# Kernel tuning notes

Hardware: AMD Instinct MI355X
Metric: run time of the kernel (lower is better)

The kernel has to match this reference:

```python
import jax, jax.numpy as jnp
import numpy as np


def setup_inputs() -> dict:
    key = jax.random.key(0)
    k1, k2 = jax.random.split(key)
    label = jax.random.normal(k1, (8, 19, 320, 2048), dtype=jnp.float32)
    energy = jax.random.normal(k2, (8, 1280, 1280), dtype=jnp.float32)
    return {"label": label, "energy": energy}


def reference(label, energy):
    b, c, h, w = label.shape
    # log_softmax over channel dim (as in original)
    ls = jax.nn.log_softmax(label, axis=1)
    hh, ww = h // 16, w // 16
    # AdaptiveAvgPool2d((h/16, w/16)) with divisible dims == exact 16x16 block mean
    pooled = ls.reshape(b, c, hh, 16, ww, 16).mean(axis=(3, 5))  # [b,c,hh,ww]
    lab = jnp.argmax(pooled, axis=1)            # [b,hh,ww]
    lab = lab[:, 10:20, :].reshape(b, -1)        # [b,P] with P = 10*ww
    # pairwise label equality mask, replacing the nested CPU loops
    same = lab[:, :, None] == lab[:, None, :]    # [b,P,P] bool
    e = jnp.where((~same) & (energy > 0), jnp.float32(-0.5), energy)
    e = jnp.where(same & (e < 0), jnp.float32(0.5), e)
    attention_map = jax.nn.softmax(e, axis=-1)
    return e, attention_map
```

## Files before the change

kernel.cpp:

```cpp
#include <hip/hip_runtime.h>
#include <math.h>

#define NC 19
#define H  320
#define W  2048
#define HW (H * W)
#define P  1280
#define NB 8

__global__ __launch_bounds__(256) void pool_argmax_kernel(
    const float* __restrict__ label, int* __restrict__ lab)
{
    int gw   = blockIdx.x * 4 + (threadIdx.x >> 6);
    int lane = threadIdx.x & 63;

    int wp = gw & 63;
    int t  = gw >> 6;
    int hp = t % 10;
    int b  = t / 10;

    int h0 = (hp + 10) * 16;
    int w0 = wp * 32;

    int r  = lane >> 3;
    int c4 = lane & 7;

    const float* p0 = label + (size_t)b * NC * HW + (size_t)(h0 + r) * W
                    + (size_t)w0 + (size_t)c4 * 4;

    float best  = -3.4e38f;
    int   bestc = 0;
    for (int c = 0; c < NC; ++c) {
        const float* pc = p0 + (size_t)c * HW;
        float4 v0 = *(const float4*)(pc);
        float4 v1 = *(const float4*)(pc + 8 * W);
        float s = ((v0.x + v0.y) + (v0.z + v0.w))
                + ((v1.x + v1.y) + (v1.z + v1.w));
        s += __shfl_xor(s, 1, 64);
        s += __shfl_xor(s, 2, 64);
        s += __shfl_xor(s, 8, 64);
        s += __shfl_xor(s, 16, 64);
        s += __shfl_xor(s, 32, 64);
        if (s > best) { best = s; bestc = c; }
    }
    if (lane == 0) lab[t * 128 + wp * 2]     = bestc;
    if (lane == 4) lab[t * 128 + wp * 2 + 1] = bestc;
}

__global__ __launch_bounds__(320) void e_softmax_kernel(
    const float* __restrict__ energy, const int* __restrict__ lab,
    float* __restrict__ e_out, float* __restrict__ attn_out)
{
    int row = blockIdx.x;
    int t   = threadIdx.x;
    int b   = row / P;
    int i   = row - b * P;

    int li = lab[b * P + i];
    int4   lj = ((const int4*)(lab + b * P))[t];
    float4 en = ((const float4*)(energy + (size_t)row * P))[t];

    int   lv[4] = { lj.x, lj.y, lj.z, lj.w };
    float ev[4] = { en.x, en.y, en.z, en.w };
    float v[4];
    #pragma unroll
    for (int m = 0; m < 4; ++m) {
        bool same = (lv[m] == li);
        v[m] = same ? (ev[m] < 0.f ?  0.5f : ev[m])
                    : (ev[m] > 0.f ? -0.5f : ev[m]);
    }

    float mx = fmaxf(fmaxf(v[0], v[1]), fmaxf(v[2], v[3]));
    #pragma unroll
    for (int off = 32; off; off >>= 1)
        mx = fmaxf(mx, __shfl_xor(mx, off, 64));
    __shared__ float redmax[5];
    __shared__ float redsum[5];
    int wv = t >> 6;
    if ((t & 63) == 0) redmax[wv] = mx;
    __syncthreads();
    mx = fmaxf(fmaxf(fmaxf(redmax[0], redmax[1]),
                     fmaxf(redmax[2], redmax[3])), redmax[4]);

    float ex[4];
    float s = 0.f;
    #pragma unroll
    for (int m = 0; m < 4; ++m) { ex[m] = __expf(v[m] - mx); s += ex[m]; }
    #pragma unroll
    for (int off = 32; off; off >>= 1)
        s += __shfl_xor(s, off, 64);
    if ((t & 63) == 0) redsum[wv] = s;
    __syncthreads();
    s = (redsum[0] + redsum[1]) + (redsum[2] + redsum[3]) + redsum[4];
    float inv = 1.0f / s;

    float4 eo = make_float4(v[0], v[1], v[2], v[3]);
    float4 ao = make_float4(ex[0] * inv, ex[1] * inv, ex[2] * inv, ex[3] * inv);
    ((float4*)(e_out    + (size_t)row * P))[t] = eo;
    ((float4*)(attn_out + (size_t)row * P))[t] = ao;
}

extern "C" void kernel_launch(void* const* d_in, const int* in_sizes, int n_in,
                              void* d_out, int out_size, void* d_ws, size_t ws_size,
                              hipStream_t stream) {
    const float* label  = (const float*)d_in[0];
    const float* energy = (const float*)d_in[1];

    float* e_out    = (float*)d_out;
    float* attn_out = e_out + (size_t)NB * P * P;
    int*   lab      = (int*)d_ws;

    hipLaunchKernelGGL(pool_argmax_kernel, dim3(1280), dim3(256), 0, stream,
                       label, lab);
    hipLaunchKernelGGL(e_softmax_kernel, dim3(NB * P), dim3(320), 0, stream,
                       energy, lab, e_out, attn_out);
}
```

Before: 525.9 us.

## Use one wavefront per softmax row and batch channel loads in pooling

The softmax kernel now gives each row to a single 64-lane wavefront that handles 20 elements per lane. This replaces the 320-thread block and its two shared-memory barrier reductions with pure shuffle reductions. The pooling kernel now issues all 19 channel loads before doing the shuffle reductions, which lets more memory requests be in flight at once. In exchange both kernels hold more registers per thread, which may lower occupancy.

```diff
diff --git a/kernel.cpp b/kernel.cpp
--- a/kernel.cpp
+++ b/kernel.cpp
@@ -28,14 +28,21 @@
     const float* p0 = label + (size_t)b * NC * HW + (size_t)(h0 + r) * W
                     + (size_t)w0 + (size_t)c4 * 4;
 
-    float best  = -3.4e38f;
-    int   bestc = 0;
+    float sc[NC];
+    #pragma unroll
     for (int c = 0; c < NC; ++c) {
         const float* pc = p0 + (size_t)c * HW;
         float4 v0 = *(const float4*)(pc);
         float4 v1 = *(const float4*)(pc + 8 * W);
-        float s = ((v0.x + v0.y) + (v0.z + v0.w))
-                + ((v1.x + v1.y) + (v1.z + v1.w));
+        sc[c] = ((v0.x + v0.y) + (v0.z + v0.w))
+              + ((v1.x + v1.y) + (v1.z + v1.w));
+    }
+
+    float best  = -3.4e38f;
+    int   bestc = 0;
+    #pragma unroll
+    for (int c = 0; c < NC; ++c) {
+        float s = sc[c];
         s += __shfl_xor(s, 1, 64);
         s += __shfl_xor(s, 2, 64);
         s += __shfl_xor(s, 8, 64);
@@ -47,57 +54,59 @@
     if (lane == 4) lab[t * 128 + wp * 2 + 1] = bestc;
 }
 
-__global__ __launch_bounds__(320) void e_softmax_kernel(
+__global__ __launch_bounds__(256) void e_softmax_kernel(
     const float* __restrict__ energy, const int* __restrict__ lab,
     float* __restrict__ e_out, float* __restrict__ attn_out)
 {
-    int row = blockIdx.x;
-    int t   = threadIdx.x;
-    int b   = row / P;
-    int i   = row - b * P;
+    int row  = blockIdx.x * 4 + (threadIdx.x >> 6);
+    int lane = threadIdx.x & 63;
+    int b = row / P;
+    int i = row - b * P;
 
     int li = lab[b * P + i];
-    int4   lj = ((const int4*)(lab + b * P))[t];
-    float4 en = ((const float4*)(energy + (size_t)row * P))[t];
+    const int4*   lrow = (const int4*)(lab + b * P);
+    const float4* erow = (const float4*)(energy + (size_t)row * P);
 
-    int   lv[4] = { lj.x, lj.y, lj.z, lj.w };
-    float ev[4] = { en.x, en.y, en.z, en.w };
-    float v[4];
+    float v[20];
+    float mx = -3.4e38f;
     #pragma unroll
-    for (int m = 0; m < 4; ++m) {
-        bool same = (lv[m] == li);
-        v[m] = same ? (ev[m] < 0.f ?  0.5f : ev[m])
-                    : (ev[m] > 0.f ? -0.5f : ev[m]);
+    for (int k = 0; k < 5; ++k) {
+        int idx = lane + 64 * k;
+        int4   lj = lrow[idx];
+        float4 en = erow[idx];
+        int   lv[4] = { lj.x, lj.y, lj.z, lj.w };
+        float ev[4] = { en.x, en.y, en.z, en.w };
+        #pragma unroll
+        for (int m = 0; m < 4; ++m) {
+            bool same = (lv[m] == li);
+            float x = same ? (ev[m] < 0.f ?  0.5f : ev[m])
+                           : (ev[m] > 0.f ? -0.5f : ev[m]);
+            v[4 * k + m] = x;
+            mx = fmaxf(mx, x);
+        }
     }
-
-    float mx = fmaxf(fmaxf(v[0], v[1]), fmaxf(v[2], v[3]));
     #pragma unroll
     for (int off = 32; off; off >>= 1)
         mx = fmaxf(mx, __shfl_xor(mx, off, 64));
-    __shared__ float redmax[5];
-    __shared__ float redsum[5];
-    int wv = t >> 6;
-    if ((t & 63) == 0) redmax[wv] = mx;
-    __syncthreads();
-    mx = fmaxf(fmaxf(fmaxf(redmax[0], redmax[1]),
-                     fmaxf(redmax[2], redmax[3])), redmax[4]);
 
-    float ex[4];
+    float ex[20];
     float s = 0.f;
     #pragma unroll
-    for (int m = 0; m < 4; ++m) { ex[m] = __expf(v[m] - mx); s += ex[m]; }
+    for (int n = 0; n < 20; ++n) { ex[n] = __expf(v[n] - mx); s += ex[n]; }
     #pragma unroll
     for (int off = 32; off; off >>= 1)
         s += __shfl_xor(s, off, 64);
-    if ((t & 63) == 0) redsum[wv] = s;
-    __syncthreads();
-    s = (redsum[0] + redsum[1]) + (redsum[2] + redsum[3]) + redsum[4];
     float inv = 1.0f / s;
 
-    float4 eo = make_float4(v[0], v[1], v[2], v[3]);
-    float4 ao = make_float4(ex[0] * inv, ex[1] * inv, ex[2] * inv, ex[3] * inv);
-    ((float4*)(e_out    + (size_t)row * P))[t] = eo;
-    ((float4*)(attn_out + (size_t)row * P))[t] = ao;
+    float4* eo = (float4*)(e_out    + (size_t)row * P);
+    float4* ao = (float4*)(attn_out + (size_t)row * P);
+    #pragma unroll
+    for (int k = 0; k < 5; ++k) {
+        int idx = lane + 64 * k;
+        eo[idx] = make_float4(v[4*k], v[4*k+1], v[4*k+2], v[4*k+3]);
+        ao[idx] = make_float4(ex[4*k] * inv, ex[4*k+1] * inv,
+                              ex[4*k+2] * inv, ex[4*k+3] * inv);
+    }
 }
 
 extern "C" void kernel_launch(void* const* d_in, const int* in_sizes, int n_in,
@@ -112,6 +121,6 @@
 
     hipLaunchKernelGGL(pool_argmax_kernel, dim3(1280), dim3(256), 0, stream,
                        label, lab);
-    hipLaunchKernelGGL(e_softmax_kernel, dim3(NB * P), dim3(320), 0, stream,
+    hipLaunchKernelGGL(e_softmax_kernel, dim3(NB * P / 4), dim3(256), 0, stream,
                        energy, lab, e_out, attn_out);
 }
```

Result: no change. 535.9 us (+1.9%).
